# Optimization experiments

Measured on AMD Instinct MI355X. Metric: run time of the kernel, lower is better.

## Reference

```python
import jax, jax.numpy as jnp
import numpy as np

LAMBDA = 1.0


def _sq_dists(x, y):
    # x: (B,N,3), y: (B,M,3) -> (B,N,M) squared euclidean distances
    x2 = jnp.sum(x * x, axis=-1)  # (B,N)
    y2 = jnp.sum(y * y, axis=-1)  # (B,M)
    xy = jnp.einsum('bnd,bmd->bnm', x, y)  # (B,N,M)
    return x2[:, :, None] + y2[:, None, :] - 2.0 * xy


def setup_inputs() -> dict:
    key = jax.random.key(0)
    k1, k2, k3 = jax.random.split(key, 3)
    B, N = 4, 8192
    pc_pred = jax.random.normal(k1, (B, N, 3), dtype=jnp.float32)
    pc_target = jax.random.normal(k2, (B, N, 3), dtype=jnp.float32)
    fbpp = jax.random.uniform(k3, (1,), dtype=jnp.float32)
    return {"pc_pred": pc_pred, "pc_target": pc_target, "fbpp": fbpp}


def reference(pc_pred, pc_target, fbpp):
    # Chamfer distance (pytorch3d semantics): squared L2 1-NN both directions,
    # mean over points, mean over batch, summed over the two directions.
    d2 = _sq_dists(pc_pred, pc_target)  # (B,N,M)
    cham_x = jnp.mean(jnp.min(d2, axis=2), axis=1)  # (B,) pred -> target
    cham_y = jnp.mean(jnp.min(d2, axis=1), axis=1)  # (B,) target -> pred
    dist = jnp.mean(cham_x) + jnp.mean(cham_y)
    rate = jnp.mean(fbpp)
    loss = dist + LAMBDA * rate
    return (loss, dist, rate)
```

## Files before the change

kernel.cpp:

```cpp
#include <hip/hip_runtime.h>
#include <math.h>

typedef _Float16 f16x8 __attribute__((ext_vector_type(8)));
typedef __fp16   fp16v2 __attribute__((ext_vector_type(2)));
typedef float    f32x16 __attribute__((ext_vector_type(16)));

#define THREADS 256
#define YCHUNK  4096
#define XPB     128

static __device__ inline unsigned pk2(float a, float b) {
    fp16v2 h = __builtin_amdgcn_cvt_pkrtz(a, b);
    return __builtin_bit_cast(unsigned, h);
}

static __device__ inline void packwrite(uint2* dst, float4 f0, float4 f1,
                                        float4 f2) {
    float n0 = fmaf(f0.x, f0.x, fmaf(f0.y, f0.y, f0.z * f0.z));
    float n1 = fmaf(f0.w, f0.w, fmaf(f1.x, f1.x, f1.y * f1.y));
    float n2 = fmaf(f1.z, f1.z, fmaf(f1.w, f1.w, f2.x * f2.x));
    float n3 = fmaf(f2.y, f2.y, fmaf(f2.z, f2.z, f2.w * f2.w));
    dst[0] = make_uint2(pk2(f0.x, f0.y), pk2(f0.z, n0));
    dst[1] = make_uint2(pk2(f0.w, f1.x), pk2(f1.y, n1));
    dst[2] = make_uint2(pk2(f1.z, f1.w), pk2(f2.x, n2));
    dst[3] = make_uint2(pk2(f2.y, f2.z), pk2(f2.w, n3));
}

__global__ __launch_bounds__(THREADS, 2) void chamfer_kernel(
    const float* __restrict__ pred, const float* __restrict__ targ,
    float* __restrict__ partials, int N)
{
    const int dir = blockIdx.z;
    const float* xsrc = dir == 0 ? pred : targ;
    const float* ysrc = dir == 0 ? targ : pred;
    const int b = blockIdx.y;

    __shared__ uint2 sy[YCHUNK];
    __shared__ float swave[4];

    const int tid  = threadIdx.x;
    const int lane = tid & 63;
    const int wave = tid >> 6;
    const int col  = lane & 31;

    const size_t xi = (size_t)(b * N + blockIdx.x * XPB + wave * 32 + col) * 3;
    const float x0 = xsrc[xi], x1 = xsrc[xi + 1], x2 = xsrc[xi + 2];

    const bool act = lane < 32;
    f16x8 bf;
    bf[0] = act ? (_Float16)(-2.0f * x0) : (_Float16)0.0f;
    bf[1] = act ? (_Float16)(-2.0f * x1) : (_Float16)0.0f;
    bf[2] = act ? (_Float16)(-2.0f * x2) : (_Float16)0.0f;
    bf[3] = act ? (_Float16)1.0f : (_Float16)0.0f;
    bf[4] = bf[5] = bf[6] = bf[7] = (_Float16)0.0f;

    f32x16 zacc;
    f32x16 vmin;
#pragma unroll
    for (int r = 0; r < 16; ++r) { zacc[r] = 0.0f; vmin[r] = INFINITY; }

#define MF(X)                                                              \
    __builtin_amdgcn_mfma_f32_32x32x16_f16(                                \
        __builtin_bit_cast(f16x8, make_uint4((X).x, (X).y, 0u, 0u)),       \
        bf, zacc, 0, 0, 0)

#define FOLD(A0, A1)                                                       \
    {                                                                      \
        _Pragma("unroll")                                                  \
        for (int r = 0; r < 16; ++r) {                                     \
            float t_;                                                      \
            asm("v_min3_f32 %0, %1, %2, %3"                                \
                : "=v"(t_)                                                 \
                : "v"(vmin[r]), "v"((A0)[r]), "v"((A1)[r]));               \
            vmin[r] = t_;                                                  \
        }                                                                  \
    }

    const int nchunks = N / YCHUNK;
    for (int c = 0; c < nchunks; ++c) {
        __syncthreads();
        {
            const float4* yf4 = (const float4*)(ysrc + (size_t)b * N * 3
                                                + (size_t)c * YCHUNK * 3);
#pragma unroll
            for (int k = 0; k < 4; ++k) {
                const int fb = k * THREADS * 3 + tid * 3;
                packwrite(&sy[(k * THREADS + tid) * 4], yf4[fb], yf4[fb + 1],
                          yf4[fb + 2]);
            }
        }
        __syncthreads();

        uint2 la0 = sy[0 * 32 + col], la1 = sy[1 * 32 + col];
        f32x16 aa0 = MF(la0), aa1 = MF(la1);
        for (int g = 2; g <= 122; g += 4) {
            uint2 lb0 = sy[(g + 0) * 32 + col];
            uint2 lb1 = sy[(g + 1) * 32 + col];
            f32x16 ab0 = MF(lb0), ab1 = MF(lb1);
            FOLD(aa0, aa1);
            uint2 lc0 = sy[(g + 2) * 32 + col];
            uint2 lc1 = sy[(g + 3) * 32 + col];
            aa0 = MF(lc0); aa1 = MF(lc1);
            FOLD(ab0, ab1);
        }
        {
            uint2 lb0 = sy[126 * 32 + col];
            uint2 lb1 = sy[127 * 32 + col];
            f32x16 ab0 = MF(lb0), ab1 = MF(lb1);
            FOLD(aa0, aa1);
            FOLD(ab0, ab1);
        }
    }
#undef MF
#undef FOLD

    float v = vmin[0];
#pragma unroll
    for (int r = 1; r < 16; ++r) v = fminf(v, vmin[r]);
    v = fminf(v, __shfl_xor(v, 32));
    float d = v + fmaf(x0, x0, fmaf(x1, x1, x2 * x2));

#pragma unroll
    for (int off = 16; off > 0; off >>= 1) d += __shfl_xor(d, off);
    if (lane == 0) swave[wave] = d;
    __syncthreads();
    if (tid == 0) {
        float s = swave[0] + swave[1] + swave[2] + swave[3];
        int bid = blockIdx.x + gridDim.x * (blockIdx.y + gridDim.y * blockIdx.z);
        partials[bid] = s;
    }
}

__global__ __launch_bounds__(512) void finalize(
    const float* __restrict__ partials, const float* __restrict__ fbpp,
    float* __restrict__ out, int nPartials, int totalPts)
{
    __shared__ float sw[8];
    const int tid = threadIdx.x;
    float v = (tid < nPartials) ? partials[tid] : 0.0f;
#pragma unroll
    for (int off = 32; off > 0; off >>= 1) v += __shfl_xor(v, off);
    if ((tid & 63) == 0) sw[tid >> 6] = v;
    __syncthreads();
    if (tid == 0) {
        float t = 0.0f;
#pragma unroll
        for (int w = 0; w < 8; ++w) t += sw[w];
        float dist = t / (float)totalPts;
        float rate = fbpp[0];
        out[0] = dist + rate;
        out[1] = dist;
        out[2] = rate;
    }
}

extern "C" void kernel_launch(void* const* d_in, const int* in_sizes, int n_in,
                              void* d_out, int out_size, void* d_ws, size_t ws_size,
                              hipStream_t stream) {
    const float* pred = (const float*)d_in[0];
    const float* targ = (const float*)d_in[1];
    const float* fbpp = (const float*)d_in[2];
    float* out = (float*)d_out;

    const int B = 4;
    const int N = in_sizes[0] / (B * 3);
    float* partials = (float*)d_ws;

    dim3 grid(N / XPB, B, 2);
    chamfer_kernel<<<grid, THREADS, 0, stream>>>(pred, targ, partials, N);

    const int nPartials = (N / XPB) * B * 2;
    finalize<<<1, 512, 0, stream>>>(partials, fbpp, out, nPartials, B * N);
}
```

Measured before the change: 24.93 us.

## Split Y chunk across wave pairs and reuse each LDS load for two X tiles

Each wave now handles two 32-point X tiles (low and high) against half of the Y chunk, so every LDS read of Y feeds two MFMAs instead of one. The per-wave minima for the two halves of Y are combined through shared memory before the sum reduction. This is meant to halve LDS read traffic per MFMA. In exchange it doubles the accumulator and minimum registers per wave, uses plain fminf instead of the inline min3 asm, and drops the explicit software pipelining of the MFMA and fold steps.

```diff
diff --git a/kernel.cpp b/kernel.cpp
--- a/kernel.cpp
+++ b/kernel.cpp
@@ -36,45 +36,46 @@
     const int b = blockIdx.y;
 
     __shared__ uint2 sy[YCHUNK];
-    __shared__ float swave[4];
+    __shared__ float sdm[2][XPB];
+    __shared__ float swave[2];
 
     const int tid  = threadIdx.x;
     const int lane = tid & 63;
     const int wave = tid >> 6;
+    const int cs   = wave & 1;
+    const int h    = wave >> 1;
     const int col  = lane & 31;
 
-    const size_t xi = (size_t)(b * N + blockIdx.x * XPB + wave * 32 + col) * 3;
-    const float x0 = xsrc[xi], x1 = xsrc[xi + 1], x2 = xsrc[xi + 2];
+    const int    xb  = blockIdx.x * XPB + cs * 64 + col;
+    const size_t xiL = (size_t)(b * N + xb) * 3;
+    const size_t xiH = (size_t)(b * N + xb + 32) * 3;
+    const float xl0 = xsrc[xiL], xl1 = xsrc[xiL + 1], xl2 = xsrc[xiL + 2];
+    const float xh0 = xsrc[xiH], xh1 = xsrc[xiH + 1], xh2 = xsrc[xiH + 2];
 
     const bool act = lane < 32;
-    f16x8 bf;
-    bf[0] = act ? (_Float16)(-2.0f * x0) : (_Float16)0.0f;
-    bf[1] = act ? (_Float16)(-2.0f * x1) : (_Float16)0.0f;
-    bf[2] = act ? (_Float16)(-2.0f * x2) : (_Float16)0.0f;
-    bf[3] = act ? (_Float16)1.0f : (_Float16)0.0f;
-    bf[4] = bf[5] = bf[6] = bf[7] = (_Float16)0.0f;
+    f16x8 bfl, bfh;
+    bfl[0] = act ? (_Float16)(-2.0f * xl0) : (_Float16)0.0f;
+    bfl[1] = act ? (_Float16)(-2.0f * xl1) : (_Float16)0.0f;
+    bfl[2] = act ? (_Float16)(-2.0f * xl2) : (_Float16)0.0f;
+    bfl[3] = act ? (_Float16)1.0f : (_Float16)0.0f;
+    bfl[4] = bfl[5] = bfl[6] = bfl[7] = (_Float16)0.0f;
+    bfh[0] = act ? (_Float16)(-2.0f * xh0) : (_Float16)0.0f;
+    bfh[1] = act ? (_Float16)(-2.0f * xh1) : (_Float16)0.0f;
+    bfh[2] = act ? (_Float16)(-2.0f * xh2) : (_Float16)0.0f;
+    bfh[3] = act ? (_Float16)1.0f : (_Float16)0.0f;
+    bfh[4] = bfh[5] = bfh[6] = bfh[7] = (_Float16)0.0f;
 
     f32x16 zacc;
-    f32x16 vmin;
+    f32x16 vmin0, vmin1;
 #pragma unroll
-    for (int r = 0; r < 16; ++r) { zacc[r] = 0.0f; vmin[r] = INFINITY; }
+    for (int r = 0; r < 16; ++r) {
+        zacc[r] = 0.0f; vmin0[r] = INFINITY; vmin1[r] = INFINITY;
+    }
 
-#define MF(X)                                                              \
+#define MF(X, BF)                                                          \
     __builtin_amdgcn_mfma_f32_32x32x16_f16(                                \
         __builtin_bit_cast(f16x8, make_uint4((X).x, (X).y, 0u, 0u)),       \
-        bf, zacc, 0, 0, 0)
-
-#define FOLD(A0, A1)                                                       \
-    {                                                                      \
-        _Pragma("unroll")                                                  \
-        for (int r = 0; r < 16; ++r) {                                     \
-            float t_;                                                      \
-            asm("v_min3_f32 %0, %1, %2, %3"                                \
-                : "=v"(t_)                                                 \
-                : "v"(vmin[r]), "v"((A0)[r]), "v"((A1)[r]));               \
-            vmin[r] = t_;                                                  \
-        }                                                                  \
-    }
+        BF, zacc, 0, 0, 0)
 
     const int nchunks = N / YCHUNK;
     for (int c = 0; c < nchunks; ++c) {
@@ -91,43 +92,49 @@
         }
         __syncthreads();
 
-        uint2 la0 = sy[0 * 32 + col], la1 = sy[1 * 32 + col];
-        f32x16 aa0 = MF(la0), aa1 = MF(la1);
-        for (int g = 2; g <= 122; g += 4) {
-            uint2 lb0 = sy[(g + 0) * 32 + col];
-            uint2 lb1 = sy[(g + 1) * 32 + col];
-            f32x16 ab0 = MF(lb0), ab1 = MF(lb1);
-            FOLD(aa0, aa1);
-            uint2 lc0 = sy[(g + 2) * 32 + col];
-            uint2 lc1 = sy[(g + 3) * 32 + col];
-            aa0 = MF(lc0); aa1 = MF(lc1);
-            FOLD(ab0, ab1);
-        }
-        {
-            uint2 lb0 = sy[126 * 32 + col];
-            uint2 lb1 = sy[127 * 32 + col];
-            f32x16 ab0 = MF(lb0), ab1 = MF(lb1);
-            FOLD(aa0, aa1);
-            FOLD(ab0, ab1);
+        const int gb = h * 64;
+        for (int g = 0; g < 64; g += 2) {
+            uint2 a0 = sy[(gb + g) * 32 + col];
+            uint2 a1 = sy[(gb + g + 1) * 32 + col];
+            f32x16 m0 = MF(a0, bfl);
+            f32x16 m1 = MF(a1, bfl);
+            f32x16 m2 = MF(a0, bfh);
+            f32x16 m3 = MF(a1, bfh);
+#pragma unroll
+            for (int r = 0; r < 16; ++r) {
+                vmin0[r] = fminf(fminf(vmin0[r], m0[r]), m1[r]);
+                vmin1[r] = fminf(fminf(vmin1[r], m2[r]), m3[r]);
+            }
         }
     }
 #undef MF
-#undef FOLD
 
-    float v = vmin[0];
+    float v0 = vmin0[0], v1 = vmin1[0];
 #pragma unroll
-    for (int r = 1; r < 16; ++r) v = fminf(v, vmin[r]);
-    v = fminf(v, __shfl_xor(v, 32));
-    float d = v + fmaf(x0, x0, fmaf(x1, x1, x2 * x2));
+    for (int r = 1; r < 16; ++r) {
+        v0 = fminf(v0, vmin0[r]); v1 = fminf(v1, vmin1[r]);
+    }
+    v0 = fminf(v0, __shfl_xor(v0, 32));
+    v1 = fminf(v1, __shfl_xor(v1, 32));
+    const float dlo = v0 + fmaf(xl0, xl0, fmaf(xl1, xl1, xl2 * xl2));
+    const float dhi = v1 + fmaf(xh0, xh0, fmaf(xh1, xh1, xh2 * xh2));
 
+    if (act) {
+        sdm[h][cs * 64 + col]      = dlo;
+        sdm[h][cs * 64 + 32 + col] = dhi;
+    }
+    __syncthreads();
+
+    if (tid < 128) {
+        float m = fminf(sdm[0][tid], sdm[1][tid]);
 #pragma unroll
-    for (int off = 16; off > 0; off >>= 1) d += __shfl_xor(d, off);
-    if (lane == 0) swave[wave] = d;
+        for (int off = 32; off > 0; off >>= 1) m += __shfl_xor(m, off);
+        if ((tid & 63) == 0) swave[tid >> 6] = m;
+    }
     __syncthreads();
     if (tid == 0) {
-        float s = swave[0] + swave[1] + swave[2] + swave[3];
         int bid = blockIdx.x + gridDim.x * (blockIdx.y + gridDim.y * blockIdx.z);
-        partials[bid] = s;
+        partials[bid] = swave[0] + swave[1];
     }
 }
 
```

New measurement: 23.31 us. 6.5% less time.
